# Kernel optimization log

Hardware: AMD Instinct MI355X
Metric: run time of the kernel (lower is better)

## Reference

```python
import jax, jax.numpy as jnp
import numpy as np

MAX_RADIUS = 10.0
NUM_BASIS = 3
H = 100
C = 32  # dim(Rs_hidden) with scalar-only irreps
LEAKY_SLOPE = 0.01

def swish(v):
    return v * jax.nn.sigmoid(v)


def setup_inputs() -> dict:
    key = jax.random.key(0)
    ks = jax.random.split(key, 10)
    B, N = 4, 256
    x = jax.random.normal(ks[0], (B, N, C), dtype=jnp.float32)
    xyz = jax.random.normal(ks[1], (B, N, 3), dtype=jnp.float32) * 3.0
    mask = jax.random.randint(ks[2], (B, N), 0, 2).astype(jnp.int64)
    # radial MLP (GaussianRadialModel): basis(3) -> h(100) -> C*C path weights
    rw1 = jax.random.normal(ks[3], (NUM_BASIS, H), dtype=jnp.float32) / np.sqrt(NUM_BASIS)
    rw2 = jax.random.normal(ks[4], (H, C * C), dtype=jnp.float32) / np.sqrt(H)
    # fc3: Linear(C, C); fc2: Linear(C, 1)
    fc3_w = jax.random.normal(ks[5], (C, C), dtype=jnp.float32) / np.sqrt(C)
    fc3_b = jax.random.normal(ks[6], (C,), dtype=jnp.float32) * 0.01
    fc2_w = jax.random.normal(ks[7], (C, 1), dtype=jnp.float32) / np.sqrt(C)
    fc2_b = jax.random.normal(ks[8], (1,), dtype=jnp.float32) * 0.01
    return {"x": x, "xyz": xyz, "mask": mask, "rw1": rw1, "rw2": rw2,
            "fc3_w": fc3_w, "fc3_b": fc3_b, "fc2_w": fc2_w, "fc2_b": fc2_b}


def _normalize(v, eps=1e-6):
    mean = jnp.mean(v, axis=-1, keepdims=True)
    std = jnp.std(v, axis=-1, keepdims=True, ddof=1)  # torch std is unbiased
    return (v - mean) / (std + eps)


def reference(x, xyz, mask, rw1, rw2, fc3_w, fc3_b, fc2_w, fc2_b):
    B, N, Cc = x.shape
    # --- fc1: e3nn point convolution with Gaussian radial kernel (l=0 paths) ---
    diff = xyz[:, :, None, :] - xyz[:, None, :, :]            # [B,N,N,3]
    r = jnp.sqrt(jnp.sum(diff * diff, axis=-1) + 1e-12)       # [B,N,N]
    spacing = MAX_RADIUS / NUM_BASIS
    centers = jnp.linspace(0.0, MAX_RADIUS, NUM_BASIS, dtype=jnp.float32)
    gamma = 1.0 / spacing
    basis = jnp.exp(-gamma * (r[..., None] - centers) ** 2)   # [B,N,N,3]
    hid = swish(jnp.einsum('zabk,kh->zabh', basis, rw1))      # [B,N,N,H]
    K = jnp.einsum('zabh,hf->zabf', hid, rw2).reshape(B, N, N, Cc, Cc)  # per-pair kernel
    out = jnp.einsum('zabij,zbj->zai', K, x) / jnp.sqrt(jnp.float32(N))  # [B,N,C]
    # --- Norm(Rs_hidden): per-irrep L2 norm; for l=0 channels this is |x| ---
    out = jnp.abs(out)
    # --- mask + sum pool over points ---
    out = jnp.where(mask[..., None] == 0, 0.0, out)
    pooled = jnp.sum(out, axis=1)                             # [B,C]
    pooled = _normalize(pooled)
    # --- MLP head: leaky_relu(fc3) -> fc2 -> flatten ---
    h1 = pooled @ fc3_w + fc3_b
    h1 = jnp.where(h1 >= 0, h1, LEAKY_SLOPE * h1)
    y = h1 @ fc2_w + fc2_b                                    # [B,1]
    return y.reshape(-1)
```

## Files before the change

kernel.cpp:

```cpp
#include <hip/hip_runtime.h>
#include <math.h>

#define GAMMA 0.3f
#define WSTR  1604

typedef __bf16 bf16x8 __attribute__((ext_vector_type(8)));
typedef __bf16 bf16x4 __attribute__((ext_vector_type(4)));
typedef float  f32x4  __attribute__((ext_vector_type(4)));

__global__ __launch_bounds__(256) void k2_fused(const float* __restrict__ x,
                                                const float* __restrict__ xyz,
                                                const float* __restrict__ rw1,
                                                const float* __restrict__ rw2,
                                                float* __restrict__ part) {
    extern __shared__ char smem[];
    __bf16* Wlds = (__bf16*)smem;
    float*  rw1s = (float*)(smem + 32 * WSTR * 2);

    int bid = blockIdx.x;
    int ac = bid & 3;
    int bc = (bid >> 2) & 15;
    int z  = bid >> 6;
    int t  = threadIdx.x;
    int w  = t >> 6;
    int l  = t & 63;
    int l16 = l & 15, lg = l >> 4;

    for (int e = t; e < 300; e += 256) rw1s[e] = rw1[e];

    int a_glob = ac * 64 + w * 16 + l16;
    float ax = xyz[(z * 256 + a_glob) * 3 + 0];
    float ay = xyz[(z * 256 + a_glob) * 3 + 1];
    float az = xyz[(z * 256 + a_glob) * 3 + 2];
    float bas[4][3];
    #pragma unroll
    for (int e = 0; e < 4; ++e) {
        int b_glob = bc * 16 + lg * 4 + e;
        float dx = xyz[(z * 256 + b_glob) * 3 + 0] - ax;
        float dy = xyz[(z * 256 + b_glob) * 3 + 1] - ay;
        float dz = xyz[(z * 256 + b_glob) * 3 + 2] - az;
        float r  = sqrtf(dx * dx + dy * dy + dz * dz + 1e-12f);
        float r5 = r - 5.f, r10 = r - 10.f;
        bas[e][0] = __expf(-GAMMA * r * r);
        bas[e][1] = __expf(-GAMMA * r5 * r5);
        bas[e][2] = __expf(-GAMMA * r10 * r10);
    }

    bf16x8 xa;
    {
        int row = z * 256 + bc * 16 + l16;
        float4 v0 = *(const float4*)(x + row * 32 + lg * 4);
        float4 v1 = *(const float4*)(x + row * 32 + lg * 4 + 16);
        xa[0] = (__bf16)v0.x; xa[1] = (__bf16)v0.y; xa[2] = (__bf16)v0.z; xa[3] = (__bf16)v0.w;
        xa[4] = (__bf16)v1.x; xa[5] = (__bf16)v1.y; xa[6] = (__bf16)v1.z; xa[7] = (__bf16)v1.w;
    }
    for (int q = 0; q < 50; ++q) {
        int nt = w * 50 + q;
        int h  = nt >> 1;
        int icol = ((nt & 1) << 4) + l16;
        const float* rp = rw2 + h * 1024 + icol * 32 + lg * 4;
        float4 r0 = *(const float4*)rp;
        float4 r1 = *(const float4*)(rp + 16);
        bf16x8 rb;
        rb[0] = (__bf16)r0.x; rb[1] = (__bf16)r0.y; rb[2] = (__bf16)r0.z; rb[3] = (__bf16)r0.w;
        rb[4] = (__bf16)r1.x; rb[5] = (__bf16)r1.y; rb[6] = (__bf16)r1.z; rb[7] = (__bf16)r1.w;
        f32x4 d = {0.f, 0.f, 0.f, 0.f};
        d = __builtin_amdgcn_mfma_f32_16x16x32_bf16(xa, rb, d, 0, 0, 0);
        #pragma unroll
        for (int r = 0; r < 4; ++r) {
            int k = h * 16 + lg * 4 + r;
            Wlds[icol * WSTR + k] = (__bf16)d[r];
        }
    }
    __syncthreads();

    f32x4 acc0 = {0.f, 0.f, 0.f, 0.f};
    f32x4 acc1 = {0.f, 0.f, 0.f, 0.f};
    for (int ks = 0; ks < 50; ++ks) {
        int h0 = 2 * ks, h1 = h0 + 1;
        float u00 = rw1s[h0],       u01 = rw1s[h1];
        float u10 = rw1s[100 + h0], u11 = rw1s[100 + h1];
        float u20 = rw1s[200 + h0], u21 = rw1s[200 + h1];
        bf16x8 af;
        #pragma unroll
        for (int e = 0; e < 4; ++e) {
            float p0 = bas[e][0] * u00 + bas[e][1] * u10 + bas[e][2] * u20;
            float p1 = bas[e][0] * u01 + bas[e][1] * u11 + bas[e][2] * u21;
            float s0 = p0 * __builtin_amdgcn_rcpf(1.f + __expf(-p0));
            float s1 = p1 * __builtin_amdgcn_rcpf(1.f + __expf(-p1));
            af[e]     = (__bf16)s0;
            af[e + 4] = (__bf16)s1;
        }
        int kb = ks * 32 + lg * 4;
        const __bf16* w0 = &Wlds[l16 * WSTR + kb];
        const __bf16* w1 = &Wlds[(16 + l16) * WSTR + kb];
        bf16x4 b0l = *(const bf16x4*)w0, b0h = *(const bf16x4*)(w0 + 16);
        bf16x4 b1l = *(const bf16x4*)w1, b1h = *(const bf16x4*)(w1 + 16);
        bf16x8 bf0 = __builtin_shufflevector(b0l, b0h, 0, 1, 2, 3, 4, 5, 6, 7);
        bf16x8 bf1 = __builtin_shufflevector(b1l, b1h, 0, 1, 2, 3, 4, 5, 6, 7);
        acc0 = __builtin_amdgcn_mfma_f32_16x16x32_bf16(af, bf0, acc0, 0, 0, 0);
        acc1 = __builtin_amdgcn_mfma_f32_16x16x32_bf16(af, bf1, acc1, 0, 0, 0);
    }

    #pragma unroll
    for (int r = 0; r < 4; ++r) {
        int a = ac * 64 + w * 16 + lg * 4 + r;
        size_t base = ((size_t)(z * 16 + bc) * 256 + a) * 32;
        part[base + l16]      = acc0[r];
        part[base + 16 + l16] = acc1[r];
    }
}

__global__ __launch_bounds__(256) void k3a_reduce(const float* __restrict__ part,
                                                  const int* __restrict__ mask,
                                                  float* __restrict__ pooled_part,
                                                  int nq) {
    int blk = blockIdx.x;
    int z = blk >> 6, ag = blk & 63;
    int t = threadIdx.x;
    int i = t & 31;
    int qg = (t >> 5) & 1;
    int a_loc = t >> 6;
    int a = ag * 4 + a_loc;
    const float* base = part + ((size_t)z * nq * 256 + (size_t)a) * 32 + i;
    float s = 0.f;
    for (int q = qg; q < nq; q += 2)
        s += base[(size_t)q * 8192];
    __shared__ float buf[4][2][32];
    buf[a_loc][qg][i] = s;
    __syncthreads();
    if (t < 128) {
        int al = t >> 5, ii = t & 31;
        float v = buf[al][0][ii] + buf[al][1][ii];
        float sc = (mask[z * 256 + ag * 4 + al] != 0) ? 0.0625f : 0.f;
        buf[al][0][ii] = fabsf(v) * sc;
    }
    __syncthreads();
    if (t < 32) {
        float v = buf[0][0][t] + buf[1][0][t] + buf[2][0][t] + buf[3][0][t];
        pooled_part[(z * 64 + ag) * 32 + t] = v;
    }
}

__global__ __launch_bounds__(128) void k3b_final(const float* __restrict__ pooled_part,
                                                 const float* __restrict__ fc3_w,
                                                 const float* __restrict__ fc3_b,
                                                 const float* __restrict__ fc2_w,
                                                 const float* __restrict__ fc2_b,
                                                 float* __restrict__ out) {
    int t = threadIdx.x;
    int z = t >> 5, i = t & 31;
    float s = 0.f;
    for (int ag = 0; ag < 64; ++ag) s += pooled_part[(z * 64 + ag) * 32 + i];
    float sm = s;
    #pragma unroll
    for (int off = 16; off; off >>= 1) sm += __shfl_xor(sm, off, 32);
    float mean = sm * (1.f / 32.f);
    float d = s - mean;
    float ss = d * d;
    #pragma unroll
    for (int off = 16; off; off >>= 1) ss += __shfl_xor(ss, off, 32);
    float stdv = sqrtf(ss * (1.f / 31.f));
    float nv = d / (stdv + 1e-6f);
    __shared__ float pn[4][32];
    pn[z][i] = nv;
    __syncthreads();
    float h1 = fc3_b[i];
    #pragma unroll
    for (int j = 0; j < 32; ++j) h1 += pn[z][j] * fc3_w[j * 32 + i];
    h1 = (h1 >= 0.f) ? h1 : 0.01f * h1;
    float y = h1 * fc2_w[i];
    #pragma unroll
    for (int off = 16; off; off >>= 1) y += __shfl_xor(y, off, 32);
    if (i == 0) out[z] = y + fc2_b[0];
}

extern "C" void kernel_launch(void* const* d_in, const int* in_sizes, int n_in,
                              void* d_out, int out_size, void* d_ws, size_t ws_size,
                              hipStream_t stream) {
    const float* x    = (const float*)d_in[0];
    const float* xyz  = (const float*)d_in[1];
    const int*   mask = (const int*)d_in[2];
    const float* rw1  = (const float*)d_in[3];
    const float* rw2  = (const float*)d_in[4];
    const float* fc3w = (const float*)d_in[5];
    const float* fc3b = (const float*)d_in[6];
    const float* fc2w = (const float*)d_in[7];
    const float* fc2b = (const float*)d_in[8];
    float* out = (float*)d_out;

    float* part        = (float*)d_ws;
    float* pooled_part = (float*)((char*)d_ws + 2097152);

    const int LDS_BYTES = 32 * WSTR * 2 + 304 * 4;

    hipLaunchKernelGGL(k2_fused,   dim3(256), dim3(256), LDS_BYTES, stream, x, xyz, rw1, rw2, part);
    hipLaunchKernelGGL(k3a_reduce, dim3(256), dim3(256), 0, stream, part, mask, pooled_part, 16);
    hipLaunchKernelGGL(k3b_final,  dim3(1),   dim3(128), 0, stream, pooled_part, fc3w, fc3b, fc2w, fc2b, out);
}
```

Before: 36.37 us.

## Split W precompute into separate kernel and halve hidden dim per block

Moves the per-(batch, b-chunk) W = x·rw2 computation out of the fused kernel into a new pre-kernel that writes bf16 W to global memory in an MFMA-friendly layout. The fused kernel now splits the hidden dimension in two, doubling the grid to 512 blocks with half the LDS each, loads W with vectorized copies, and reads B fragments as single 8-wide loads. Previously each of the 4 a-chunk blocks recomputed the same W, so this removes that redundancy and raises occupancy. The cost is an extra launch, a global round-trip of about 6.5 MB, and twice as many partial sums for the reduction kernel.

```diff
diff --git a/kernel.cpp b/kernel.cpp
--- a/kernel.cpp
+++ b/kernel.cpp
@@ -2,31 +2,72 @@
 #include <math.h>
 
 #define GAMMA 0.3f
-#define WSTR  1604
+#define WSTR  808
 
 typedef __bf16 bf16x8 __attribute__((ext_vector_type(8)));
 typedef __bf16 bf16x4 __attribute__((ext_vector_type(4)));
 typedef float  f32x4  __attribute__((ext_vector_type(4)));
 
-__global__ __launch_bounds__(256) void k2_fused(const float* __restrict__ x,
+__global__ __launch_bounds__(256) void k1_W(const float* __restrict__ x,
+                                            const float* __restrict__ rw2,
+                                            __bf16* __restrict__ Wg) {
+    int bid = blockIdx.x;
+    int mt = bid / 25, nq = bid % 25;
+    int z = mt >> 4, bc = mt & 15;
+    int t = threadIdx.x, w = t >> 6, l = t & 63;
+    int l16 = l & 15, lg = l >> 4;
+
+    int row = (z * 256 + bc * 16 + l16) * 32;
+    float4 v0 = *(const float4*)(x + row + lg * 4);
+    float4 v1 = *(const float4*)(x + row + lg * 4 + 16);
+    bf16x8 xa;
+    xa[0] = (__bf16)v0.x; xa[1] = (__bf16)v0.y; xa[2] = (__bf16)v0.z; xa[3] = (__bf16)v0.w;
+    xa[4] = (__bf16)v1.x; xa[5] = (__bf16)v1.y; xa[6] = (__bf16)v1.z; xa[7] = (__bf16)v1.w;
+
+    #pragma unroll
+    for (int q = 0; q < 2; ++q) {
+        int nt = nq * 8 + w * 2 + q;
+        int h = nt >> 1, hpar = h & 1, hp = h >> 1;
+        int icol = ((nt & 1) << 4) + l16;
+        const float* rp = rw2 + h * 1024 + icol * 32 + lg * 4;
+        float4 r0 = *(const float4*)rp;
+        float4 r1 = *(const float4*)(rp + 16);
+        bf16x8 rb;
+        rb[0] = (__bf16)r0.x; rb[1] = (__bf16)r0.y; rb[2] = (__bf16)r0.z; rb[3] = (__bf16)r0.w;
+        rb[4] = (__bf16)r1.x; rb[5] = (__bf16)r1.y; rb[6] = (__bf16)r1.z; rb[7] = (__bf16)r1.w;
+        f32x4 d = {0.f, 0.f, 0.f, 0.f};
+        d = __builtin_amdgcn_mfma_f32_16x16x32_bf16(xa, rb, d, 0, 0, 0);
+        bf16x4 pk;
+        pk[0] = (__bf16)d[0]; pk[1] = (__bf16)d[1]; pk[2] = (__bf16)d[2]; pk[3] = (__bf16)d[3];
+        size_t off = ((size_t)((z * 16 + bc) * 50 + hp) * 32 + icol) * 32 + lg * 8 + hpar * 4;
+        *(bf16x4*)(Wg + off) = pk;
+    }
+}
+
+__global__ __launch_bounds__(256) void k2_fused(const __bf16* __restrict__ Wg,
                                                 const float* __restrict__ xyz,
                                                 const float* __restrict__ rw1,
-                                                const float* __restrict__ rw2,
                                                 float* __restrict__ part) {
-    extern __shared__ char smem[];
-    __bf16* Wlds = (__bf16*)smem;
-    float*  rw1s = (float*)(smem + 32 * WSTR * 2);
+    __shared__ __bf16 Wlds[32 * WSTR];
+    __shared__ float rw1s[304];
 
     int bid = blockIdx.x;
     int ac = bid & 3;
-    int bc = (bid >> 2) & 15;
-    int z  = bid >> 6;
-    int t  = threadIdx.x;
-    int w  = t >> 6;
-    int l  = t & 63;
+    int hh = (bid >> 2) & 1;
+    int bc = (bid >> 3) & 15;
+    int z  = bid >> 7;
+    int t  = threadIdx.x, w = t >> 6, l = t & 63;
     int l16 = l & 15, lg = l >> 4;
 
     for (int e = t; e < 300; e += 256) rw1s[e] = rw1[e];
+
+    const __bf16* gsrc = Wg + ((size_t)((z * 16 + bc) * 50 + hh * 25)) * 1024;
+    for (int c = t; c < 3200; c += 256) {
+        int hp = c >> 7, rem = c & 127;
+        int i = rem >> 2, kq = rem & 3;
+        uint4 v = *(const uint4*)(gsrc + c * 8);
+        *(uint4*)&Wlds[i * WSTR + hp * 32 + kq * 8] = v;
+    }
 
     int a_glob = ac * 64 + w * 16 + l16;
     float ax = xyz[(z * 256 + a_glob) * 3 + 0];
@@ -45,39 +86,12 @@
         bas[e][1] = __expf(-GAMMA * r5 * r5);
         bas[e][2] = __expf(-GAMMA * r10 * r10);
     }
-
-    bf16x8 xa;
-    {
-        int row = z * 256 + bc * 16 + l16;
-        float4 v0 = *(const float4*)(x + row * 32 + lg * 4);
-        float4 v1 = *(const float4*)(x + row * 32 + lg * 4 + 16);
-        xa[0] = (__bf16)v0.x; xa[1] = (__bf16)v0.y; xa[2] = (__bf16)v0.z; xa[3] = (__bf16)v0.w;
-        xa[4] = (__bf16)v1.x; xa[5] = (__bf16)v1.y; xa[6] = (__bf16)v1.z; xa[7] = (__bf16)v1.w;
-    }
-    for (int q = 0; q < 50; ++q) {
-        int nt = w * 50 + q;
-        int h  = nt >> 1;
-        int icol = ((nt & 1) << 4) + l16;
-        const float* rp = rw2 + h * 1024 + icol * 32 + lg * 4;
-        float4 r0 = *(const float4*)rp;
-        float4 r1 = *(const float4*)(rp + 16);
-        bf16x8 rb;
-        rb[0] = (__bf16)r0.x; rb[1] = (__bf16)r0.y; rb[2] = (__bf16)r0.z; rb[3] = (__bf16)r0.w;
-        rb[4] = (__bf16)r1.x; rb[5] = (__bf16)r1.y; rb[6] = (__bf16)r1.z; rb[7] = (__bf16)r1.w;
-        f32x4 d = {0.f, 0.f, 0.f, 0.f};
-        d = __builtin_amdgcn_mfma_f32_16x16x32_bf16(xa, rb, d, 0, 0, 0);
-        #pragma unroll
-        for (int r = 0; r < 4; ++r) {
-            int k = h * 16 + lg * 4 + r;
-            Wlds[icol * WSTR + k] = (__bf16)d[r];
-        }
-    }
     __syncthreads();
 
     f32x4 acc0 = {0.f, 0.f, 0.f, 0.f};
     f32x4 acc1 = {0.f, 0.f, 0.f, 0.f};
-    for (int ks = 0; ks < 50; ++ks) {
-        int h0 = 2 * ks, h1 = h0 + 1;
+    for (int ks = 0; ks < 25; ++ks) {
+        int h0 = hh * 50 + 2 * ks, h1 = h0 + 1;
         float u00 = rw1s[h0],       u01 = rw1s[h1];
         float u10 = rw1s[100 + h0], u11 = rw1s[100 + h1];
         float u20 = rw1s[200 + h0], u21 = rw1s[200 + h1];
@@ -91,21 +105,18 @@
             af[e]     = (__bf16)s0;
             af[e + 4] = (__bf16)s1;
         }
-        int kb = ks * 32 + lg * 4;
-        const __bf16* w0 = &Wlds[l16 * WSTR + kb];
-        const __bf16* w1 = &Wlds[(16 + l16) * WSTR + kb];
-        bf16x4 b0l = *(const bf16x4*)w0, b0h = *(const bf16x4*)(w0 + 16);
-        bf16x4 b1l = *(const bf16x4*)w1, b1h = *(const bf16x4*)(w1 + 16);
-        bf16x8 bf0 = __builtin_shufflevector(b0l, b0h, 0, 1, 2, 3, 4, 5, 6, 7);
-        bf16x8 bf1 = __builtin_shufflevector(b1l, b1h, 0, 1, 2, 3, 4, 5, 6, 7);
+        const __bf16* w0 = &Wlds[l16 * WSTR + ks * 32 + lg * 8];
+        bf16x8 bf0 = *(const bf16x8*)w0;
+        bf16x8 bf1 = *(const bf16x8*)(w0 + 16 * WSTR);
         acc0 = __builtin_amdgcn_mfma_f32_16x16x32_bf16(af, bf0, acc0, 0, 0, 0);
         acc1 = __builtin_amdgcn_mfma_f32_16x16x32_bf16(af, bf1, acc1, 0, 0, 0);
     }
 
+    int qc = bc * 2 + hh;
     #pragma unroll
     for (int r = 0; r < 4; ++r) {
         int a = ac * 64 + w * 16 + lg * 4 + r;
-        size_t base = ((size_t)(z * 16 + bc) * 256 + a) * 32;
+        size_t base = ((size_t)(z * 32 + qc) * 256 + a) * 32;
         part[base + l16]      = acc0[r];
         part[base + 16 + l16] = acc1[r];
     }
@@ -113,8 +124,7 @@
 
 __global__ __launch_bounds__(256) void k3a_reduce(const float* __restrict__ part,
                                                   const int* __restrict__ mask,
-                                                  float* __restrict__ pooled_part,
-                                                  int nq) {
+                                                  float* __restrict__ pooled_part) {
     int blk = blockIdx.x;
     int z = blk >> 6, ag = blk & 63;
     int t = threadIdx.x;
@@ -122,9 +132,9 @@
     int qg = (t >> 5) & 1;
     int a_loc = t >> 6;
     int a = ag * 4 + a_loc;
-    const float* base = part + ((size_t)z * nq * 256 + (size_t)a) * 32 + i;
+    const float* base = part + ((size_t)z * 32 * 256 + (size_t)a) * 32 + i;
     float s = 0.f;
-    for (int q = qg; q < nq; q += 2)
+    for (int q = qg; q < 32; q += 2)
         s += base[(size_t)q * 8192];
     __shared__ float buf[4][2][32];
     buf[a_loc][qg][i] = s;
@@ -189,12 +199,12 @@
     const float* fc2b = (const float*)d_in[8];
     float* out = (float*)d_out;
 
-    float* part        = (float*)d_ws;
-    float* pooled_part = (float*)((char*)d_ws + 2097152);
-
-    const int LDS_BYTES = 32 * WSTR * 2 + 304 * 4;
-
-    hipLaunchKernelGGL(k2_fused,   dim3(256), dim3(256), LDS_BYTES, stream, x, xyz, rw1, rw2, part);
-    hipLaunchKernelGGL(k3a_reduce, dim3(256), dim3(256), 0, stream, part, mask, pooled_part, 16);
-    hipLaunchKernelGGL(k3b_final,  dim3(1),   dim3(128), 0, stream, pooled_part, fc3w, fc3b, fc2w, fc2b, out);
-}
+    __bf16* Wg         = (__bf16*)d_ws;
+    float*  part       = (float*)((char*)d_ws + 6553600);
+    float*  pooled_part= (float*)((char*)d_ws + 6553600 + 4194304);
+
+    hipLaunchKernelGGL(k1_W,       dim3(1600), dim3(256), 0, stream, x, rw2, Wg);
+    hipLaunchKernelGGL(k2_fused,   dim3(512),  dim3(256), 0, stream, Wg, xyz, rw1, part);
+    hipLaunchKernelGGL(k3a_reduce, dim3(256),  dim3(256), 0, stream, part, mask, pooled_part);
+    hipLaunchKernelGGL(k3b_final,  dim3(1),    dim3(128), 0, stream, pooled_part, fc3w, fc3b, fc2w, fc2b, out);
+}
```

Measured after the change: 40.48 us. 11.3% more time.

## Split hidden dimension across two waves per row tile with LDS reduction

Applied to the files above, without the earlier changes.

Doubles the k2_fused block to 512 threads and splits the 100-wide hidden reduction between two waves per 16-row tile, combining their partial accumulators through a padded LDS buffer before writing. The weight-building phase is spread over 8 waves (25 tiles each) and writes packed bf16x4 stores instead of scalar stores, with the LDS row stride changed to keep those stores aligned. This shortens the serial per-wave chain of swish and MFMA work, at the cost of an extra barrier, more LDS, and fewer concurrent blocks per CU.

```diff
diff --git a/kernel.cpp b/kernel.cpp
--- a/kernel.cpp
+++ b/kernel.cpp
@@ -2,13 +2,13 @@
 #include <math.h>
 
 #define GAMMA 0.3f
-#define WSTR  1604
+#define WSTR  1608
 
 typedef __bf16 bf16x8 __attribute__((ext_vector_type(8)));
 typedef __bf16 bf16x4 __attribute__((ext_vector_type(4)));
 typedef float  f32x4  __attribute__((ext_vector_type(4)));
 
-__global__ __launch_bounds__(256) void k2_fused(const float* __restrict__ x,
+__global__ __launch_bounds__(512) void k2_fused(const float* __restrict__ x,
                                                 const float* __restrict__ xyz,
                                                 const float* __restrict__ rw1,
                                                 const float* __restrict__ rw2,
@@ -16,6 +16,7 @@
     extern __shared__ char smem[];
     __bf16* Wlds = (__bf16*)smem;
     float*  rw1s = (float*)(smem + 32 * WSTR * 2);
+    float (*red)[2][16][17] = (float(*)[2][16][17])(smem + 32 * WSTR * 2 + 1216);
 
     int bid = blockIdx.x;
     int ac = bid & 3;
@@ -23,12 +24,13 @@
     int z  = bid >> 6;
     int t  = threadIdx.x;
     int w  = t >> 6;
+    int wa = w >> 1, wk = w & 1;
     int l  = t & 63;
     int l16 = l & 15, lg = l >> 4;
 
-    for (int e = t; e < 300; e += 256) rw1s[e] = rw1[e];
-
-    int a_glob = ac * 64 + w * 16 + l16;
+    for (int e = t; e < 300; e += 512) rw1s[e] = rw1[e];
+
+    int a_glob = ac * 64 + wa * 16 + l16;
     float ax = xyz[(z * 256 + a_glob) * 3 + 0];
     float ay = xyz[(z * 256 + a_glob) * 3 + 1];
     float az = xyz[(z * 256 + a_glob) * 3 + 2];
@@ -48,14 +50,14 @@
 
     bf16x8 xa;
     {
-        int row = z * 256 + bc * 16 + l16;
-        float4 v0 = *(const float4*)(x + row * 32 + lg * 4);
-        float4 v1 = *(const float4*)(x + row * 32 + lg * 4 + 16);
+        int row = (z * 256 + bc * 16 + l16) * 32;
+        float4 v0 = *(const float4*)(x + row + lg * 4);
+        float4 v1 = *(const float4*)(x + row + lg * 4 + 16);
         xa[0] = (__bf16)v0.x; xa[1] = (__bf16)v0.y; xa[2] = (__bf16)v0.z; xa[3] = (__bf16)v0.w;
         xa[4] = (__bf16)v1.x; xa[5] = (__bf16)v1.y; xa[6] = (__bf16)v1.z; xa[7] = (__bf16)v1.w;
     }
-    for (int q = 0; q < 50; ++q) {
-        int nt = w * 50 + q;
+    for (int q = 0; q < 25; ++q) {
+        int nt = w * 25 + q;
         int h  = nt >> 1;
         int icol = ((nt & 1) << 4) + l16;
         const float* rp = rw2 + h * 1024 + icol * 32 + lg * 4;
@@ -66,18 +68,17 @@
         rb[4] = (__bf16)r1.x; rb[5] = (__bf16)r1.y; rb[6] = (__bf16)r1.z; rb[7] = (__bf16)r1.w;
         f32x4 d = {0.f, 0.f, 0.f, 0.f};
         d = __builtin_amdgcn_mfma_f32_16x16x32_bf16(xa, rb, d, 0, 0, 0);
-        #pragma unroll
-        for (int r = 0; r < 4; ++r) {
-            int k = h * 16 + lg * 4 + r;
-            Wlds[icol * WSTR + k] = (__bf16)d[r];
-        }
+        bf16x4 pk;
+        pk[0] = (__bf16)d[0]; pk[1] = (__bf16)d[1]; pk[2] = (__bf16)d[2]; pk[3] = (__bf16)d[3];
+        *(bf16x4*)&Wlds[icol * WSTR + h * 16 + lg * 4] = pk;
     }
     __syncthreads();
 
     f32x4 acc0 = {0.f, 0.f, 0.f, 0.f};
     f32x4 acc1 = {0.f, 0.f, 0.f, 0.f};
-    for (int ks = 0; ks < 50; ++ks) {
-        int h0 = 2 * ks, h1 = h0 + 1;
+    for (int ks = 0; ks < 25; ++ks) {
+        int hp = wk * 25 + ks;
+        int h0 = 2 * hp, h1 = h0 + 1;
         float u00 = rw1s[h0],       u01 = rw1s[h1];
         float u10 = rw1s[100 + h0], u11 = rw1s[100 + h1];
         float u20 = rw1s[200 + h0], u21 = rw1s[200 + h1];
@@ -91,9 +92,9 @@
             af[e]     = (__bf16)s0;
             af[e + 4] = (__bf16)s1;
         }
-        int kb = ks * 32 + lg * 4;
+        int kb = hp * 32 + lg * 4;
         const __bf16* w0 = &Wlds[l16 * WSTR + kb];
-        const __bf16* w1 = &Wlds[(16 + l16) * WSTR + kb];
+        const __bf16* w1 = w0 + 16 * WSTR;
         bf16x4 b0l = *(const bf16x4*)w0, b0h = *(const bf16x4*)(w0 + 16);
         bf16x4 b1l = *(const bf16x4*)w1, b1h = *(const bf16x4*)(w1 + 16);
         bf16x8 bf0 = __builtin_shufflevector(b0l, b0h, 0, 1, 2, 3, 4, 5, 6, 7);
@@ -102,19 +103,30 @@
         acc1 = __builtin_amdgcn_mfma_f32_16x16x32_bf16(af, bf1, acc1, 0, 0, 0);
     }
 
-    #pragma unroll
-    for (int r = 0; r < 4; ++r) {
-        int a = ac * 64 + w * 16 + lg * 4 + r;
-        size_t base = ((size_t)(z * 16 + bc) * 256 + a) * 32;
-        part[base + l16]      = acc0[r];
-        part[base + 16 + l16] = acc1[r];
+    if (wk == 1) {
+        #pragma unroll
+        for (int r = 0; r < 4; ++r) {
+            red[wa][0][lg * 4 + r][l16] = acc0[r];
+            red[wa][1][lg * 4 + r][l16] = acc1[r];
+        }
+    }
+    __syncthreads();
+    if (wk == 0) {
+        #pragma unroll
+        for (int r = 0; r < 4; ++r) {
+            float v0 = acc0[r] + red[wa][0][lg * 4 + r][l16];
+            float v1 = acc1[r] + red[wa][1][lg * 4 + r][l16];
+            int a = ac * 64 + wa * 16 + lg * 4 + r;
+            size_t base = ((size_t)(z * 16 + bc) * 256 + a) * 32;
+            part[base + l16]      = v0;
+            part[base + 16 + l16] = v1;
+        }
     }
 }
 
 __global__ __launch_bounds__(256) void k3a_reduce(const float* __restrict__ part,
                                                   const int* __restrict__ mask,
-                                                  float* __restrict__ pooled_part,
-                                                  int nq) {
+                                                  float* __restrict__ pooled_part) {
     int blk = blockIdx.x;
     int z = blk >> 6, ag = blk & 63;
     int t = threadIdx.x;
@@ -122,9 +134,9 @@
     int qg = (t >> 5) & 1;
     int a_loc = t >> 6;
     int a = ag * 4 + a_loc;
-    const float* base = part + ((size_t)z * nq * 256 + (size_t)a) * 32 + i;
+    const float* base = part + ((size_t)z * 16 * 256 + (size_t)a) * 32 + i;
     float s = 0.f;
-    for (int q = qg; q < nq; q += 2)
+    for (int q = qg; q < 16; q += 2)
         s += base[(size_t)q * 8192];
     __shared__ float buf[4][2][32];
     buf[a_loc][qg][i] = s;
@@ -192,9 +204,9 @@
     float* part        = (float*)d_ws;
     float* pooled_part = (float*)((char*)d_ws + 2097152);
 
-    const int LDS_BYTES = 32 * WSTR * 2 + 304 * 4;
-
-    hipLaunchKernelGGL(k2_fused,   dim3(256), dim3(256), LDS_BYTES, stream, x, xyz, rw1, rw2, part);
-    hipLaunchKernelGGL(k3a_reduce, dim3(256), dim3(256), 0, stream, part, mask, pooled_part, 16);
+    const int LDS_BYTES = 32 * WSTR * 2 + 1216 + 8704;
+
+    hipLaunchKernelGGL(k2_fused,   dim3(256), dim3(512), LDS_BYTES, stream, x, xyz, rw1, rw2, part);
+    hipLaunchKernelGGL(k3a_reduce, dim3(256), dim3(256), 0, stream, part, mask, pooled_part);
     hipLaunchKernelGGL(k3b_final,  dim3(1),   dim3(128), 0, stream, pooled_part, fc3w, fc3b, fc2w, fc2b, out);
 }
```

After: 34.92 us. -4.0%, faster.

## Split hidden dimension across four blocks to quadruple grid and shrink LDS

Applied to the files above, without the earlier changes.

The main kernel's hidden dimension (100) is split into four chunks of 25. The grid grows from 256 to 1024 blocks, each holding a much smaller LDS weight tile, and the partial-sum buffer grows fourfold with the reduction covering 64 partials instead of 16. The LDS layout is reorganised so each B fragment is read with one 8-element vector load, and the odd 25th hidden unit is handled by a zero-padded final MFMA step. This targets low occupancy on the 256-CU device at the cost of four times the partial-output traffic and a longer reduction.

```diff
diff --git a/kernel.cpp b/kernel.cpp
--- a/kernel.cpp
+++ b/kernel.cpp
@@ -2,33 +2,37 @@
 #include <math.h>
 
 #define GAMMA 0.3f
-#define WSTR  1604
+#define WSTR3 424
 
 typedef __bf16 bf16x8 __attribute__((ext_vector_type(8)));
 typedef __bf16 bf16x4 __attribute__((ext_vector_type(4)));
 typedef float  f32x4  __attribute__((ext_vector_type(4)));
 
-__global__ __launch_bounds__(256) void k2_fused(const float* __restrict__ x,
-                                                const float* __restrict__ xyz,
-                                                const float* __restrict__ rw1,
-                                                const float* __restrict__ rw2,
-                                                float* __restrict__ part) {
-    extern __shared__ char smem[];
-    __bf16* Wlds = (__bf16*)smem;
-    float*  rw1s = (float*)(smem + 32 * WSTR * 2);
+__global__ __launch_bounds__(256, 4) void k2_fused(const float* __restrict__ x,
+                                                   const float* __restrict__ xyz,
+                                                   const float* __restrict__ rw1,
+                                                   const float* __restrict__ rw2,
+                                                   float* __restrict__ part) {
+    __shared__ __bf16 Wlds[32 * WSTR3];
+    __shared__ float  rw1s[304];
 
     int bid = blockIdx.x;
-    int ac = bid & 3;
-    int bc = (bid >> 2) & 15;
-    int z  = bid >> 6;
+    int ah = bid & 3;
+    int hh = (bid >> 2) & 3;
+    int bc = (bid >> 4) & 15;
+    int z  = bid >> 8;
     int t  = threadIdx.x;
     int w  = t >> 6;
     int l  = t & 63;
     int l16 = l & 15, lg = l >> 4;
 
     for (int e = t; e < 300; e += 256) rw1s[e] = rw1[e];
-
-    int a_glob = ac * 64 + w * 16 + l16;
+    if (t < 128) {
+        int icol = t >> 2, g = t & 3;
+        *(bf16x4*)&Wlds[icol * WSTR3 + 12 * 32 + g * 8 + 4] = (bf16x4){(__bf16)0.f, (__bf16)0.f, (__bf16)0.f, (__bf16)0.f};
+    }
+
+    int a_glob = ah * 64 + w * 16 + l16;
     float ax = xyz[(z * 256 + a_glob) * 3 + 0];
     float ay = xyz[(z * 256 + a_glob) * 3 + 1];
     float az = xyz[(z * 256 + a_glob) * 3 + 2];
@@ -48,39 +52,41 @@
 
     bf16x8 xa;
     {
-        int row = z * 256 + bc * 16 + l16;
-        float4 v0 = *(const float4*)(x + row * 32 + lg * 4);
-        float4 v1 = *(const float4*)(x + row * 32 + lg * 4 + 16);
+        int row = (z * 256 + bc * 16 + l16) * 32;
+        float4 v0 = *(const float4*)(x + row + lg * 4);
+        float4 v1 = *(const float4*)(x + row + lg * 4 + 16);
         xa[0] = (__bf16)v0.x; xa[1] = (__bf16)v0.y; xa[2] = (__bf16)v0.z; xa[3] = (__bf16)v0.w;
         xa[4] = (__bf16)v1.x; xa[5] = (__bf16)v1.y; xa[6] = (__bf16)v1.z; xa[7] = (__bf16)v1.w;
     }
-    for (int q = 0; q < 50; ++q) {
-        int nt = w * 50 + q;
-        int h  = nt >> 1;
-        int icol = ((nt & 1) << 4) + l16;
-        const float* rp = rw2 + h * 1024 + icol * 32 + lg * 4;
-        float4 r0 = *(const float4*)rp;
-        float4 r1 = *(const float4*)(rp + 16);
-        bf16x8 rb;
-        rb[0] = (__bf16)r0.x; rb[1] = (__bf16)r0.y; rb[2] = (__bf16)r0.z; rb[3] = (__bf16)r0.w;
-        rb[4] = (__bf16)r1.x; rb[5] = (__bf16)r1.y; rb[6] = (__bf16)r1.z; rb[7] = (__bf16)r1.w;
-        f32x4 d = {0.f, 0.f, 0.f, 0.f};
-        d = __builtin_amdgcn_mfma_f32_16x16x32_bf16(xa, rb, d, 0, 0, 0);
-        #pragma unroll
-        for (int r = 0; r < 4; ++r) {
-            int k = h * 16 + lg * 4 + r;
-            Wlds[icol * WSTR + k] = (__bf16)d[r];
+    for (int q = 0; q < 13; ++q) {
+        int nt = q * 4 + w;
+        if (nt < 50) {
+            int h_loc = nt >> 1;
+            int h = hh * 25 + h_loc;
+            int ks = h_loc >> 1, hpar = h_loc & 1;
+            int icol = ((nt & 1) << 4) + l16;
+            const float* rp = rw2 + h * 1024 + icol * 32 + lg * 4;
+            float4 r0 = *(const float4*)rp;
+            float4 r1 = *(const float4*)(rp + 16);
+            bf16x8 rb;
+            rb[0] = (__bf16)r0.x; rb[1] = (__bf16)r0.y; rb[2] = (__bf16)r0.z; rb[3] = (__bf16)r0.w;
+            rb[4] = (__bf16)r1.x; rb[5] = (__bf16)r1.y; rb[6] = (__bf16)r1.z; rb[7] = (__bf16)r1.w;
+            f32x4 d = {0.f, 0.f, 0.f, 0.f};
+            d = __builtin_amdgcn_mfma_f32_16x16x32_bf16(xa, rb, d, 0, 0, 0);
+            bf16x4 pk;
+            pk[0] = (__bf16)d[0]; pk[1] = (__bf16)d[1]; pk[2] = (__bf16)d[2]; pk[3] = (__bf16)d[3];
+            *(bf16x4*)&Wlds[icol * WSTR3 + ks * 32 + lg * 8 + hpar * 4] = pk;
         }
     }
     __syncthreads();
 
     f32x4 acc0 = {0.f, 0.f, 0.f, 0.f};
     f32x4 acc1 = {0.f, 0.f, 0.f, 0.f};
-    for (int ks = 0; ks < 50; ++ks) {
-        int h0 = 2 * ks, h1 = h0 + 1;
-        float u00 = rw1s[h0],       u01 = rw1s[h1];
-        float u10 = rw1s[100 + h0], u11 = rw1s[100 + h1];
-        float u20 = rw1s[200 + h0], u21 = rw1s[200 + h1];
+    for (int ks = 0; ks < 12; ++ks) {
+        int h0 = hh * 25 + 2 * ks;
+        float u00 = rw1s[h0],       u01 = rw1s[h0 + 1];
+        float u10 = rw1s[100 + h0], u11 = rw1s[101 + h0];
+        float u20 = rw1s[200 + h0], u21 = rw1s[201 + h0];
         bf16x8 af;
         #pragma unroll
         for (int e = 0; e < 4; ++e) {
@@ -91,21 +97,35 @@
             af[e]     = (__bf16)s0;
             af[e + 4] = (__bf16)s1;
         }
-        int kb = ks * 32 + lg * 4;
-        const __bf16* w0 = &Wlds[l16 * WSTR + kb];
-        const __bf16* w1 = &Wlds[(16 + l16) * WSTR + kb];
-        bf16x4 b0l = *(const bf16x4*)w0, b0h = *(const bf16x4*)(w0 + 16);
-        bf16x4 b1l = *(const bf16x4*)w1, b1h = *(const bf16x4*)(w1 + 16);
-        bf16x8 bf0 = __builtin_shufflevector(b0l, b0h, 0, 1, 2, 3, 4, 5, 6, 7);
-        bf16x8 bf1 = __builtin_shufflevector(b1l, b1h, 0, 1, 2, 3, 4, 5, 6, 7);
+        int kb = ks * 32 + lg * 8;
+        bf16x8 bf0 = *(const bf16x8*)&Wlds[l16 * WSTR3 + kb];
+        bf16x8 bf1 = *(const bf16x8*)&Wlds[(16 + l16) * WSTR3 + kb];
         acc0 = __builtin_amdgcn_mfma_f32_16x16x32_bf16(af, bf0, acc0, 0, 0, 0);
         acc1 = __builtin_amdgcn_mfma_f32_16x16x32_bf16(af, bf1, acc1, 0, 0, 0);
     }
-
+    {
+        int h0 = hh * 25 + 24;
+        float u00 = rw1s[h0], u10 = rw1s[100 + h0], u20 = rw1s[200 + h0];
+        bf16x8 af;
+        #pragma unroll
+        for (int e = 0; e < 4; ++e) {
+            float p0 = bas[e][0] * u00 + bas[e][1] * u10 + bas[e][2] * u20;
+            float s0 = p0 * __builtin_amdgcn_rcpf(1.f + __expf(-p0));
+            af[e]     = (__bf16)s0;
+            af[e + 4] = (__bf16)0.f;
+        }
+        int kb = 12 * 32 + lg * 8;
+        bf16x8 bf0 = *(const bf16x8*)&Wlds[l16 * WSTR3 + kb];
+        bf16x8 bf1 = *(const bf16x8*)&Wlds[(16 + l16) * WSTR3 + kb];
+        acc0 = __builtin_amdgcn_mfma_f32_16x16x32_bf16(af, bf0, acc0, 0, 0, 0);
+        acc1 = __builtin_amdgcn_mfma_f32_16x16x32_bf16(af, bf1, acc1, 0, 0, 0);
+    }
+
+    int qc = bc * 4 + hh;
     #pragma unroll
     for (int r = 0; r < 4; ++r) {
-        int a = ac * 64 + w * 16 + lg * 4 + r;
-        size_t base = ((size_t)(z * 16 + bc) * 256 + a) * 32;
+        int a = ah * 64 + w * 16 + lg * 4 + r;
+        size_t base = ((size_t)(z * 64 + qc) * 256 + a) * 32;
         part[base + l16]      = acc0[r];
         part[base + 16 + l16] = acc1[r];
     }
@@ -113,8 +133,7 @@
 
 __global__ __launch_bounds__(256) void k3a_reduce(const float* __restrict__ part,
                                                   const int* __restrict__ mask,
-                                                  float* __restrict__ pooled_part,
-                                                  int nq) {
+                                                  float* __restrict__ pooled_part) {
     int blk = blockIdx.x;
     int z = blk >> 6, ag = blk & 63;
     int t = threadIdx.x;
@@ -122,9 +141,9 @@
     int qg = (t >> 5) & 1;
     int a_loc = t >> 6;
     int a = ag * 4 + a_loc;
-    const float* base = part + ((size_t)z * nq * 256 + (size_t)a) * 32 + i;
+    const float* base = part + ((size_t)z * 64 * 256 + (size_t)a) * 32 + i;
     float s = 0.f;
-    for (int q = qg; q < nq; q += 2)
+    for (int q = qg; q < 64; q += 2)
         s += base[(size_t)q * 8192];
     __shared__ float buf[4][2][32];
     buf[a_loc][qg][i] = s;
@@ -190,11 +209,9 @@
     float* out = (float*)d_out;
 
     float* part        = (float*)d_ws;
-    float* pooled_part = (float*)((char*)d_ws + 2097152);
-
-    const int LDS_BYTES = 32 * WSTR * 2 + 304 * 4;
-
-    hipLaunchKernelGGL(k2_fused,   dim3(256), dim3(256), LDS_BYTES, stream, x, xyz, rw1, rw2, part);
-    hipLaunchKernelGGL(k3a_reduce, dim3(256), dim3(256), 0, stream, part, mask, pooled_part, 16);
-    hipLaunchKernelGGL(k3b_final,  dim3(1),   dim3(128), 0, stream, pooled_part, fc3w, fc3b, fc2w, fc2b, out);
-}
+    float* pooled_part = (float*)((char*)d_ws + 8388608);
+
+    hipLaunchKernelGGL(k2_fused,   dim3(1024), dim3(256), 0, stream, x, xyz, rw1, rw2, part);
+    hipLaunchKernelGGL(k3a_reduce, dim3(256),  dim3(256), 0, stream, part, mask, pooled_part);
+    hipLaunchKernelGGL(k3b_final,  dim3(1),    dim3(128), 0, stream, pooled_part, fc3w, fc3b, fc2w, fc2b, out);
+}
```

New measurement: 41.60 us. 1.14x slower.
